# Kernel tuning notes

Measured on AMD Instinct MI355X. Metric: run time of the kernel, lower is better.

The kernel has to match this reference:

```python
import jax, jax.numpy as jnp
import numpy as np

FEA_DIM = 256
NUM_HEADS = 8
B, N = 32, 48


def setup_inputs() -> dict:
    key = jax.random.key(0)
    ks = jax.random.split(key, 30)
    d = FEA_DIM
    inp = {
        "async_fea": jax.random.normal(ks[0], (B, N, d), dtype=jnp.float32),
        "sync_fea": jax.random.normal(ks[1], (B, N, d), dtype=jnp.float32),
        "async_adj": jax.random.randint(ks[2], (B, N, N), 0, 2, dtype=jnp.int32),
        "sync_adj": jax.random.randint(ks[3], (B, N, N), 0, 2, dtype=jnp.int32),
    }
    i = 4
    for pref in ("a_", "s_"):
        for nm in ("Wq", "Wk", "Wv", "Wo", "Wm"):
            inp[pref + nm] = 0.02 * jax.random.normal(ks[i], (d, d), dtype=jnp.float32); i += 1
            inp[pref + nm.replace("W", "b")] = 0.02 * jax.random.normal(ks[i], (d,), dtype=jnp.float32); i += 1
    return inp


def _aggregate(x_src, adj, fallback, Wq, bq, Wk, bk, Wv, bv, Wo, bo, Wm, bm):
    """For each target t: self-attention among neighbor set {s : adj[b,s,t] > 0}
    of x_src, mean-pool over neighbors, divide by count again, linear map.
    Targets with no neighbors fall back to `fallback`."""
    Bb, Nn, D = x_src.shape
    H = NUM_HEADS
    dh = D // H
    q = (x_src @ Wq.T + bq).reshape(Bb, Nn, H, dh)
    k = (x_src @ Wk.T + bk).reshape(Bb, Nn, H, dh)
    v = (x_src @ Wv.T + bv).reshape(Bb, Nn, H, dh)
    # shared pairwise scores among source nodes: [B, H, Q, K]
    scores = jnp.einsum("bqhd,bkhd->bhqk", q, k) / jnp.sqrt(jnp.float32(dh))
    # neighbor mask per target: adj[b, s, t] > 0 -> m[b, t, s]
    m = jnp.transpose(adj > 0, (0, 2, 1))  # [B, T, S] bool
    # per-target masked softmax over keys: logits [B, T, H, Q, K]
    key_bias = jnp.where(m[:, :, None, None, :], 0.0, -1e9)
    attn = jax.nn.softmax(scores[:, None] + key_bias, axis=-1)  # [B,T,H,Q,K]
    out = jnp.einsum("bthqk,bkhd->bthqd", attn, v).reshape(Bb, Nn, Nn, D)  # [B,T,Q,D]
    out = out @ Wo.T + bo
    mf = m.astype(out.dtype)  # [B, T, Q]
    cnt = mf.sum(-1)  # [B, T]
    denom = jnp.maximum(cnt, 1.0)
    # torch: mean over valid queries, then / edge_cnt  => sum / cnt^2
    pooled = jnp.einsum("btq,btqd->btd", mf, out) / (denom * denom)[..., None]
    mapped = pooled @ Wm.T + bm
    return jnp.where((cnt > 0)[..., None], mapped, fallback)


def reference(async_fea, sync_fea, async_adj, sync_adj,
              a_Wq, a_bq, a_Wk, a_bk, a_Wv, a_bv, a_Wo, a_bo, a_Wm, a_bm,
              s_Wq, s_bq, s_Wk, s_bk, s_Wv, s_bv, s_Wo, s_bo, s_Wm, s_bm):
    refined_async = _aggregate(sync_fea, sync_adj, async_fea,
                               a_Wq, a_bq, a_Wk, a_bk, a_Wv, a_bv, a_Wo, a_bo, a_Wm, a_bm)
    refined_sync = _aggregate(async_fea, async_adj, sync_fea,
                              s_Wq, s_bq, s_Wk, s_bk, s_Wv, s_bv, s_Wo, s_bo, s_Wm, s_bm)
    return jnp.concatenate([refined_async, refined_sync, async_fea, sync_fea], axis=2)
```

## Files before the change

### kernel.cpp

```cpp
#include <hip/hip_runtime.h>

typedef __attribute__((ext_vector_type(8))) short short8v;
typedef __attribute__((ext_vector_type(4))) float f32x4;
typedef unsigned short u16t;

__device__ __forceinline__ u16t f2bf(float f) {
    union { float f; unsigned u; } v; v.f = f;
    unsigned u = v.u;
    return (u16t)((u + 0x7FFFu + ((u >> 16) & 1u)) >> 16);
}
__device__ __forceinline__ float bf2f(u16t u) {
    union { unsigned u; float f; } v; v.u = ((unsigned)u) << 16; return v.f;
}
__device__ __forceinline__ short8v cvt8(const float* p) {
    float4 lo = *(const float4*)p;
    float4 hi = *(const float4*)(p + 4);
    union { uint4 u; short8v s; } r;
    asm("v_cvt_pk_bf16_f32 %0, %1, %2" : "=v"(r.u.x) : "v"(lo.x), "v"(lo.y));
    asm("v_cvt_pk_bf16_f32 %0, %1, %2" : "=v"(r.u.y) : "v"(lo.z), "v"(lo.w));
    asm("v_cvt_pk_bf16_f32 %0, %1, %2" : "=v"(r.u.z) : "v"(hi.x), "v"(hi.y));
    asm("v_cvt_pk_bf16_f32 %0, %1, %2" : "=v"(r.u.w) : "v"(hi.z), "v"(hi.w));
    return r.s;
}
__device__ __forceinline__ short8v ld52(const u16t* p) {
    union { uint2 u[2]; short8v s; } r;
    r.u[0] = *(const uint2*)(p);
    r.u[1] = *(const uint2*)(p + 4);
    return r.s;
}

struct Params {
    const float *async_fea, *sync_fea;
    const int *async_adj, *sync_adj;
    const float *Wf[10];
    const float *bqkv[6];
    const float *bo_[2], *bm_[2];
    u16t *Wb;
    u16t *Qb, *Kb, *Vb;
    u16t *Eg, *ETg;
    float *out;
};

__global__ __launch_bounds__(256) void convert_kernel(Params p)
{
    int g8 = (blockIdx.x * 256 + threadIdx.x) * 8;
    int w = g8 >> 16;
    int off = g8 & 65535;
    *(short8v*)(p.Wb + g8) = cvt8(p.Wf[w] + off);
}

__global__ __launch_bounds__(256) void qkv_kernel(Params p)
{
    int bid = blockIdx.x;
    int agg = bid / 288, rem = bid % 288;
    int rt = rem / 12, ct = rem % 12;
    int wave = threadIdx.x >> 6, lane = threadIdx.x & 63;
    int l15 = lane & 15, g = lane >> 4;
    int row0 = rt * 64 + wave * 16;
    int mat = ct >> 2;
    int cbase = (ct & 3) * 64;
    const float* X = agg ? p.async_fea : p.sync_fea;
    const float* Xp = X + (row0 + l15) * 256 + g * 8;
    const u16t* Wp = p.Wb + (agg * 5 + mat) * 65536 + (cbase + l15) * 256 + g * 8;
    f32x4 acc[4] = {{0,0,0,0},{0,0,0,0},{0,0,0,0},{0,0,0,0}};
    #pragma unroll
    for (int kk = 0; kk < 8; ++kk) {
        short8v a = cvt8(Xp + kk * 32);
        #pragma unroll
        for (int j = 0; j < 4; ++j) {
            short8v b = *(const short8v*)(Wp + j * 16 * 256 + kk * 32);
            acc[j] = __builtin_amdgcn_mfma_f32_16x16x32_bf16(a, b, acc[j], 0, 0, 0);
        }
    }
    const float* bias = p.bqkv[agg * 3 + mat];
    u16t* dst = ((mat == 0) ? p.Qb : (mat == 1) ? p.Kb : p.Vb) + agg * 393216;
    #pragma unroll
    for (int j = 0; j < 4; ++j) {
        int c = cbase + j * 16 + l15;
        float bv = bias[c];
        #pragma unroll
        for (int i = 0; i < 4; ++i) {
            int row = row0 + g * 4 + i;
            dst[row * 256 + c] = f2bf(acc[j][i] + bv);
        }
    }
}

__global__ __launch_bounds__(192) void scores_kernel(Params p)
{
    int bid = blockIdx.x;
    int agg = bid >> 8, r = bid & 255, b = r >> 3, h = r & 7;
    int qt = threadIdx.x >> 6, lane = threadIdx.x & 63;
    int l15 = lane & 15, g = lane >> 4;
    const u16t* Qp = p.Qb + agg * 393216 + (b * 48 + qt * 16 + l15) * 256 + h * 32 + g * 8;
    short8v a = *(const short8v*)Qp;
    f32x4 acc[3];
    #pragma unroll
    for (int kt = 0; kt < 3; ++kt) {
        const u16t* Kp = p.Kb + agg * 393216 + (b * 48 + kt * 16 + l15) * 256 + h * 32 + g * 8;
        short8v kb = *(const short8v*)Kp;
        f32x4 z = {0.f, 0.f, 0.f, 0.f};
        acc[kt] = __builtin_amdgcn_mfma_f32_16x16x32_bf16(a, kb, z, 0, 0, 0);
    }
    const float scale = 0.17677669529663687f;
    float sc[3][4], rm[4];
    #pragma unroll
    for (int i = 0; i < 4; ++i) {
        #pragma unroll
        for (int kt = 0; kt < 3; ++kt) sc[kt][i] = acc[kt][i] * scale;
        rm[i] = fmaxf(fmaxf(sc[0][i], sc[1][i]), sc[2][i]);
    }
    #pragma unroll
    for (int m = 1; m <= 8; m <<= 1)
        #pragma unroll
        for (int i = 0; i < 4; ++i) rm[i] = fmaxf(rm[i], __shfl_xor(rm[i], m));
    u16t* Eb  = p.Eg  + (agg * 32 + b) * 18432 + h * 2304;
    u16t* ETb = p.ETg + (agg * 32 + b) * 18432 + h * 2304;
    #pragma unroll
    for (int kt = 0; kt < 3; ++kt)
        #pragma unroll
        for (int i = 0; i < 4; ++i) {
            u16t ev = f2bf(__expf(sc[kt][i] - rm[i]));
            int q = qt * 16 + g * 4 + i, k = kt * 16 + l15;
            Eb[q * 48 + k]  = ev;
            ETb[k * 48 + q] = ev;
        }
}

#define VT_OFF   0
#define IV_OFF   26624
#define YV_OFF   39936
#define PL_OFF   53248
#define PO_OFF   61696
#define MSK_OFF  70144
#define CNT_OFF  71808
#define SM3_SIZE 71872
#define SP 52
#define XP 264

__global__ __launch_bounds__(512) void agg_kernel(Params p)
{
    __shared__ __attribute__((aligned(16))) char sm[SM3_SIZE];
    u16t* VT   = (u16t*)(sm + VT_OFF);
    u16t* iv_  = (u16t*)(sm + IV_OFF);
    u16t* yv_  = (u16t*)(sm + YV_OFF);
    u16t* P_l  = (u16t*)(sm + PL_OFF);
    u16t* po_  = (u16t*)(sm + PO_OFF);
    u16t* mskb = (u16t*)(sm + MSK_OFF);
    float* cnt_l = (float*)(sm + CNT_OFF);

    const int bid = blockIdx.x, tid = threadIdx.x;
    const int agg = bid >> 7, rem = bid & 127;
    const int b = rem >> 2, tg = rem & 3;
    const int wave = tid >> 6, lane = tid & 63;
    const int l15 = lane & 15, g = lane >> 4;
    const int row_base = b * 48 + tg * 12;

    const float* fb  = agg ? p.sync_fea  : p.async_fea;
    const int*   adj = agg ? p.async_adj : p.sync_adj;
    const u16t* Egb  = p.Eg  + (agg * 32 + b) * 18432;
    const u16t* ETb  = p.ETg + (agg * 32 + b) * 18432;

    #pragma unroll
    for (int l = 0; l < 3; ++l) {
        int idx = l * 4096 + tid * 8;
        int k = idx >> 8, d0 = idx & 255;
        uint4 v = *(const uint4*)(p.Vb + agg * 393216 + (b * 48 + k) * 256 + d0);
        const u16t* pv = (const u16t*)&v;
        #pragma unroll
        for (int j = 0; j < 8; ++j) VT[(d0 + j) * SP + k] = pv[j];
    }
    for (int e = tid; e < 16 * SP; e += 512) {
        int tt = e / SP, k = e - tt * SP;
        u16t v = 0;
        if (tt < 12 && k < 48)
            v = (adj[(b * 48 + k) * 48 + tg * 12 + tt] > 0) ? (u16t)0x3F80 : (u16t)0;
        mskb[e] = v;
    }
    {
        const float4* fb4 = (const float4*)fb;
        float4* out4 = (float4*)p.out;
        for (int e = tid; e < 768; e += 512) {
            int r = e >> 6, c = e & 63;
            out4[(row_base + r) * 256 + 128 + agg * 64 + c] =
                fb4[(row_base + r) * 64 + c];
        }
    }
    __syncthreads();
    if (tid < 12) {
        float c = 0.f;
        for (int s = 0; s < 48; ++s) c += bf2f(mskb[tid * SP + s]);
        cnt_l[tid] = c;
    }

    #pragma unroll
    for (int jj = 0; jj < 3; ++jj) {
        int rt = wave * 3 + jj;
        const u16t* Arow = Egb + (rt * 16 + l15) * 48;
        const u16t* Brow = mskb + l15 * SP;
        f32x4 acc = {0.f, 0.f, 0.f, 0.f};
        short8v a0 = *(const short8v*)(Arow + g * 8);
        short8v b0 = ld52(Brow + g * 8);
        acc = __builtin_amdgcn_mfma_f32_16x16x32_bf16(a0, b0, acc, 0, 0, 0);
        short8v a1 = {0,0,0,0,0,0,0,0}, b1 = {0,0,0,0,0,0,0,0};
        if (g < 2) { a1 = *(const short8v*)(Arow + 32 + g * 8); b1 = ld52(Brow + 32 + g * 8); }
        acc = __builtin_amdgcn_mfma_f32_16x16x32_bf16(a1, b1, acc, 0, 0, 0);
        #pragma unroll
        for (int i = 0; i < 4; ++i) {
            int row = rt * 16 + g * 4 + i;
            int h = row / 48, q = row - h * 48;
            float mq = bf2f(mskb[l15 * SP + q]);
            float ivv = (mq > 0.f) ? (1.f / acc[i]) : 0.f;
            iv_[(h * 16 + l15) * SP + q] = f2bf(ivv);
        }
    }
    __syncthreads();

    #pragma unroll
    for (int jj = 0; jj < 3; ++jj) {
        int job = wave * 3 + jj;
        int h = job / 3, kt = job % 3;
        const u16t* Arow = iv_ + (h * 16 + l15) * SP;
        const u16t* Brow = ETb + (h * 48 + kt * 16 + l15) * 48;
        f32x4 acc = {0.f, 0.f, 0.f, 0.f};
        short8v a0 = ld52(Arow + g * 8);
        short8v b0 = *(const short8v*)(Brow + g * 8);
        acc = __builtin_amdgcn_mfma_f32_16x16x32_bf16(a0, b0, acc, 0, 0, 0);
        short8v a1 = {0,0,0,0,0,0,0,0}, b1 = {0,0,0,0,0,0,0,0};
        if (g < 2) { a1 = ld52(Arow + 32 + g * 8); b1 = *(const short8v*)(Brow + 32 + g * 8); }
        acc = __builtin_amdgcn_mfma_f32_16x16x32_bf16(a1, b1, acc, 0, 0, 0);
        #pragma unroll
        for (int i = 0; i < 4; ++i) {
            int tt = g * 4 + i, k = kt * 16 + l15;
            float mk = bf2f(mskb[tt * SP + k]);
            yv_[(h * 16 + tt) * SP + k] = f2bf(acc[i] * mk);
        }
    }
    __syncthreads();

    #pragma unroll
    for (int jj = 0; jj < 2; ++jj) {
        int job = wave * 2 + jj;
        int h = job >> 1, dt = job & 1;
        const u16t* Arow = yv_ + (h * 16 + l15) * SP;
        const u16t* Brow = VT + (h * 32 + dt * 16 + l15) * SP;
        f32x4 acc = {0.f, 0.f, 0.f, 0.f};
        short8v a0 = ld52(Arow + g * 8), b0 = ld52(Brow + g * 8);
        acc = __builtin_amdgcn_mfma_f32_16x16x32_bf16(a0, b0, acc, 0, 0, 0);
        short8v a1 = {0,0,0,0,0,0,0,0}, b1 = {0,0,0,0,0,0,0,0};
        if (g < 2) { a1 = ld52(Arow + 32 + g * 8); b1 = ld52(Brow + 32 + g * 8); }
        acc = __builtin_amdgcn_mfma_f32_16x16x32_bf16(a1, b1, acc, 0, 0, 0);
        #pragma unroll
        for (int i = 0; i < 4; ++i)
            P_l[(g * 4 + i) * XP + h * 32 + dt * 16 + l15] = f2bf(acc[i]);
    }
    __syncthreads();

    {
        const u16t* Wo = p.Wb + (agg * 5 + 3) * 65536;
        const float* bo = p.bo_[agg];
        #pragma unroll
        for (int jj = 0; jj < 2; ++jj) {
            int ct = wave * 2 + jj;
            f32x4 acc = {0.f, 0.f, 0.f, 0.f};
            const u16t* Wp = Wo + (ct * 16 + l15) * 256 + g * 8;
            #pragma unroll
            for (int kk = 0; kk < 8; ++kk) {
                short8v a = *(const short8v*)(P_l + l15 * XP + kk * 32 + g * 8);
                short8v bf = *(const short8v*)(Wp + kk * 32);
                acc = __builtin_amdgcn_mfma_f32_16x16x32_bf16(a, bf, acc, 0, 0, 0);
            }
            int c = ct * 16 + l15;
            float bov = bo[c];
            #pragma unroll
            for (int i = 0; i < 4; ++i) {
                int t = g * 4 + i;
                float val = 0.f;
                if (t < 12) {
                    float cn = cnt_l[t];
                    float i1 = (cn > 0.f) ? 1.f / cn : 0.f;
                    val = acc[i] * i1 * i1 + bov * i1;
                }
                po_[t * XP + c] = f2bf(val);
            }
        }
    }
    __syncthreads();

    {
        const u16t* Wm = p.Wb + (agg * 5 + 4) * 65536;
        const float* bm = p.bm_[agg];
        #pragma unroll
        for (int jj = 0; jj < 2; ++jj) {
            int ct = wave * 2 + jj;
            f32x4 acc = {0.f, 0.f, 0.f, 0.f};
            const u16t* Wp = Wm + (ct * 16 + l15) * 256 + g * 8;
            #pragma unroll
            for (int kk = 0; kk < 8; ++kk) {
                short8v a = *(const short8v*)(po_ + l15 * XP + kk * 32 + g * 8);
                short8v bf = *(const short8v*)(Wp + kk * 32);
                acc = __builtin_amdgcn_mfma_f32_16x16x32_bf16(a, bf, acc, 0, 0, 0);
            }
            int c = ct * 16 + l15;
            float bmv = bm[c];
            #pragma unroll
            for (int i = 0; i < 4; ++i) {
                int t = g * 4 + i;
                if (t < 12) {
                    int grow = row_base + t;
                    float cn = cnt_l[t];
                    float val = (cn > 0.f) ? (acc[i] + bmv) : fb[grow * 256 + c];
                    p.out[grow * 1024 + agg * 256 + c] = val;
                }
            }
        }
    }
}

extern "C" void kernel_launch(void* const* d_in, const int* in_sizes, int n_in,
                              void* d_out, int out_size, void* d_ws, size_t ws_size,
                              hipStream_t stream)
{
    Params p;
    p.async_fea = (const float*)d_in[0];
    p.sync_fea  = (const float*)d_in[1];
    p.async_adj = (const int*)d_in[2];
    p.sync_adj  = (const int*)d_in[3];
    p.Wf[0] = (const float*)d_in[4];
    p.Wf[1] = (const float*)d_in[6];
    p.Wf[2] = (const float*)d_in[8];
    p.Wf[3] = (const float*)d_in[10];
    p.Wf[4] = (const float*)d_in[12];
    p.Wf[5] = (const float*)d_in[14];
    p.Wf[6] = (const float*)d_in[16];
    p.Wf[7] = (const float*)d_in[18];
    p.Wf[8] = (const float*)d_in[20];
    p.Wf[9] = (const float*)d_in[22];
    p.bqkv[0] = (const float*)d_in[5];
    p.bqkv[1] = (const float*)d_in[7];
    p.bqkv[2] = (const float*)d_in[9];
    p.bqkv[3] = (const float*)d_in[15];
    p.bqkv[4] = (const float*)d_in[17];
    p.bqkv[5] = (const float*)d_in[19];
    p.bo_[0] = (const float*)d_in[11];
    p.bo_[1] = (const float*)d_in[21];
    p.bm_[0] = (const float*)d_in[13];
    p.bm_[1] = (const float*)d_in[23];

    u16t* us = (u16t*)d_ws;
    p.Wb  = us;
    p.Qb  = p.Wb + 655360;
    p.Kb  = p.Qb + 786432;
    p.Vb  = p.Kb + 786432;
    p.Eg  = p.Vb + 786432;
    p.ETg = p.Eg + 1179648;
    p.out = (float*)d_out;

    convert_kernel<<<320, 256, 0, stream>>>(p);
    qkv_kernel<<<576, 256, 0, stream>>>(p);
    scores_kernel<<<512, 192, 0, stream>>>(p);
    agg_kernel<<<256, 512, 0, stream>>>(p);
}
```

Baseline: 52.98 us.

## Write V transposed from QKV kernel and remap blocks for XCD locality

The QKV kernel now writes V directly in a per-batch transposed [d][k] layout to global memory, so the aggregation kernel reads it straight into MFMA operands. This removes the shared-memory transpose stage and roughly halves LDS use, which may allow more blocks per CU. In addition, all three kernels remap block IDs so that blocks sharing an aggregation and batch land on the same XCD, improving L2 reuse. The cost is scattered 2-byte stores for the transposed V writes and V operand loads coming from global/L2 instead of LDS.

```diff
diff --git a/kernel.cpp b/kernel.cpp
--- a/kernel.cpp
+++ b/kernel.cpp
@@ -36,7 +36,8 @@
     const float *bqkv[6];
     const float *bo_[2], *bm_[2];
     u16t *Wb;
-    u16t *Qb, *Kb, *Vb;
+    u16t *Qb, *Kb;
+    u16t *VTg;
     u16t *Eg, *ETg;
     float *out;
 };
@@ -52,8 +53,9 @@
 __global__ __launch_bounds__(256) void qkv_kernel(Params p)
 {
     int bid = blockIdx.x;
-    int agg = bid / 288, rem = bid % 288;
-    int rt = rem / 12, ct = rem % 12;
+    int xcd = bid & 7, idx = bid >> 3;
+    int agg = xcd >> 2, xcd_in = xcd & 3;
+    int ct = idx % 12, rt = (idx / 12) * 4 + xcd_in;
     int wave = threadIdx.x >> 6, lane = threadIdx.x & 63;
     int l15 = lane & 15, g = lane >> 4;
     int row0 = rt * 64 + wave * 16;
@@ -73,15 +75,29 @@
         }
     }
     const float* bias = p.bqkv[agg * 3 + mat];
-    u16t* dst = ((mat == 0) ? p.Qb : (mat == 1) ? p.Kb : p.Vb) + agg * 393216;
-    #pragma unroll
-    for (int j = 0; j < 4; ++j) {
-        int c = cbase + j * 16 + l15;
-        float bv = bias[c];
-        #pragma unroll
-        for (int i = 0; i < 4; ++i) {
-            int row = row0 + g * 4 + i;
-            dst[row * 256 + c] = f2bf(acc[j][i] + bv);
+    if (mat < 2) {
+        u16t* dst = ((mat == 0) ? p.Qb : p.Kb) + agg * 393216;
+        #pragma unroll
+        for (int j = 0; j < 4; ++j) {
+            int c = cbase + j * 16 + l15;
+            float bv = bias[c];
+            #pragma unroll
+            for (int i = 0; i < 4; ++i) {
+                int row = row0 + g * 4 + i;
+                dst[row * 256 + c] = f2bf(acc[j][i] + bv);
+            }
+        }
+    } else {
+        u16t* vt = p.VTg + agg * 393216;
+        #pragma unroll
+        for (int j = 0; j < 4; ++j) {
+            int c = cbase + j * 16 + l15;
+            float bv = bias[c];
+            #pragma unroll
+            for (int i = 0; i < 4; ++i) {
+                int row = row0 + g * 4 + i;
+                vt[(row / 48) * 12288 + c * 48 + (row % 48)] = f2bf(acc[j][i] + bv);
+            }
         }
     }
 }
@@ -89,7 +105,9 @@
 __global__ __launch_bounds__(192) void scores_kernel(Params p)
 {
     int bid = blockIdx.x;
-    int agg = bid >> 8, r = bid & 255, b = r >> 3, h = r & 7;
+    int xcd = bid & 7, idx = bid >> 3;
+    int agg = xcd >> 2, xcd_in = xcd & 3;
+    int h = idx & 7, b = (idx >> 3) * 4 + xcd_in;
     int qt = threadIdx.x >> 6, lane = threadIdx.x & 63;
     int l15 = lane & 15, g = lane >> 4;
     const u16t* Qp = p.Qb + agg * 393216 + (b * 48 + qt * 16 + l15) * 256 + h * 32 + g * 8;
@@ -127,21 +145,19 @@
         }
 }
 
-#define VT_OFF   0
-#define IV_OFF   26624
-#define YV_OFF   39936
-#define PL_OFF   53248
-#define PO_OFF   61696
-#define MSK_OFF  70144
-#define CNT_OFF  71808
-#define SM3_SIZE 71872
+#define IV_OFF   0
+#define YV_OFF   13312
+#define PL_OFF   26624
+#define MSK_OFF  35072
+#define CNT_OFF  36736
+#define SM3_SIZE 36800
+#define PO_OFF   IV_OFF
 #define SP 52
 #define XP 264
 
 __global__ __launch_bounds__(512) void agg_kernel(Params p)
 {
     __shared__ __attribute__((aligned(16))) char sm[SM3_SIZE];
-    u16t* VT   = (u16t*)(sm + VT_OFF);
     u16t* iv_  = (u16t*)(sm + IV_OFF);
     u16t* yv_  = (u16t*)(sm + YV_OFF);
     u16t* P_l  = (u16t*)(sm + PL_OFF);
@@ -150,8 +166,9 @@
     float* cnt_l = (float*)(sm + CNT_OFF);
 
     const int bid = blockIdx.x, tid = threadIdx.x;
-    const int agg = bid >> 7, rem = bid & 127;
-    const int b = rem >> 2, tg = rem & 3;
+    const int xcd = bid & 7, idx = bid >> 3;
+    const int agg = xcd >> 2, xcd_in = xcd & 3;
+    const int tg = idx >> 3, b = ((idx & 7) << 2) | xcd_in;
     const int wave = tid >> 6, lane = tid & 63;
     const int l15 = lane & 15, g = lane >> 4;
     const int row_base = b * 48 + tg * 12;
@@ -160,16 +177,8 @@
     const int*   adj = agg ? p.async_adj : p.sync_adj;
     const u16t* Egb  = p.Eg  + (agg * 32 + b) * 18432;
     const u16t* ETb  = p.ETg + (agg * 32 + b) * 18432;
-
-    #pragma unroll
-    for (int l = 0; l < 3; ++l) {
-        int idx = l * 4096 + tid * 8;
-        int k = idx >> 8, d0 = idx & 255;
-        uint4 v = *(const uint4*)(p.Vb + agg * 393216 + (b * 48 + k) * 256 + d0);
-        const u16t* pv = (const u16t*)&v;
-        #pragma unroll
-        for (int j = 0; j < 8; ++j) VT[(d0 + j) * SP + k] = pv[j];
-    }
+    const u16t* VTb  = p.VTg + agg * 393216 + b * 12288;
+
     for (int e = tid; e < 16 * SP; e += 512) {
         int tt = e / SP, k = e - tt * SP;
         u16t v = 0;
@@ -243,12 +252,13 @@
         int job = wave * 2 + jj;
         int h = job >> 1, dt = job & 1;
         const u16t* Arow = yv_ + (h * 16 + l15) * SP;
-        const u16t* Brow = VT + (h * 32 + dt * 16 + l15) * SP;
+        const u16t* Brow = VTb + (h * 32 + dt * 16 + l15) * 48;
         f32x4 acc = {0.f, 0.f, 0.f, 0.f};
-        short8v a0 = ld52(Arow + g * 8), b0 = ld52(Brow + g * 8);
+        short8v a0 = ld52(Arow + g * 8);
+        short8v b0 = *(const short8v*)(Brow + g * 8);
         acc = __builtin_amdgcn_mfma_f32_16x16x32_bf16(a0, b0, acc, 0, 0, 0);
         short8v a1 = {0,0,0,0,0,0,0,0}, b1 = {0,0,0,0,0,0,0,0};
-        if (g < 2) { a1 = ld52(Arow + 32 + g * 8); b1 = ld52(Brow + 32 + g * 8); }
+        if (g < 2) { a1 = ld52(Arow + 32 + g * 8); b1 = *(const short8v*)(Brow + 32 + g * 8); }
         acc = __builtin_amdgcn_mfma_f32_16x16x32_bf16(a1, b1, acc, 0, 0, 0);
         #pragma unroll
         for (int i = 0; i < 4; ++i)
@@ -351,8 +361,8 @@
     p.Wb  = us;
     p.Qb  = p.Wb + 655360;
     p.Kb  = p.Qb + 786432;
-    p.Vb  = p.Kb + 786432;
-    p.Eg  = p.Vb + 786432;
+    p.VTg = p.Kb + 786432;
+    p.Eg  = p.VTg + 786432;
     p.ETg = p.Eg + 1179648;
     p.out = (float*)d_out;
 
```

After: 50.75 us (median of 2 runs). 1.04x faster.
